# Performance work log

Measured on AMD Instinct MI355X. Metric: run time of the kernel, lower is better.

## Reference

```python
import jax, jax.numpy as jnp
import numpy as np

HIDDEN = 2048
NUM_HEADS = 6
HEAD_V = 512          # head_dim * expand_v = 256 * 2
VALUE_DIM = NUM_HEADS * HEAD_V  # 3072
CONV_K = 4
PHASE_BASE = 10000.0
EPS = 1e-5


def _causal_depthwise_conv(x, w):
    # x: [B, T, C], w: [C, K]; causal depthwise conv, no bias, no activation
    B, T, C = x.shape
    K = w.shape[1]
    xp = jnp.pad(x, ((0, 0), (K - 1, 0), (0, 0)))
    y = jnp.zeros_like(x)
    for j in range(K):
        y = y + xp[:, j:j + T, :] * w[:, j]
    return y


def _rotate(x, ang):
    # x: [..., D] interleaved RoPE pairs, ang: [..., D//2] pair angles
    cos = jnp.cos(ang)
    sin = jnp.sin(ang)
    xe = x[..., ::2]
    xo = x[..., 1::2]
    ye = xe * cos - xo * sin
    yo = xo * cos + xe * sin
    return jnp.stack([ye, yo], axis=-1).reshape(x.shape)


def setup_inputs() -> dict:
    key = jax.random.key(0)
    ks = jax.random.split(key, 12)
    s = 0.02
    return {
        "hidden_states": jax.random.normal(ks[0], (2, 2048, HIDDEN), jnp.float32),
        "Wq": jax.random.normal(ks[1], (HIDDEN, VALUE_DIM), jnp.float32) * s,
        "Wk": jax.random.normal(ks[2], (HIDDEN, VALUE_DIM), jnp.float32) * s,
        "Wv": jax.random.normal(ks[3], (HIDDEN, VALUE_DIM), jnp.float32) * s,
        "Wa": jax.random.normal(ks[4], (HIDDEN, NUM_HEADS), jnp.float32) * s,
        "Wb": jax.random.normal(ks[5], (HIDDEN, NUM_HEADS), jnp.float32) * s,
        "Wg": jax.random.normal(ks[6], (HIDDEN, VALUE_DIM), jnp.float32) * s,
        "Wo": jax.random.normal(ks[7], (VALUE_DIM, HIDDEN), jnp.float32) * s,
        "conv_q": jax.random.normal(ks[8], (VALUE_DIM, CONV_K), jnp.float32) * s,
        "conv_k": jax.random.normal(ks[9], (VALUE_DIM, CONV_K), jnp.float32) * s,
        "conv_v": jax.random.normal(ks[10], (VALUE_DIM, CONV_K), jnp.float32) * s,
        "rms_w": jnp.ones((HEAD_V,), jnp.float32),
    }


def _forward(hidden_states, Wq, Wk, Wv, Wa, Wb, Wg, Wo, conv_q, conv_k, conv_v, rms_w):
    B, T, _ = hidden_states.shape
    H, D = NUM_HEADS, HEAD_V
    inv_freq = 1.0 / (PHASE_BASE ** (jnp.arange(0, D, 2, dtype=jnp.float32) / D))  # [D/2]

    q = _causal_depthwise_conv(hidden_states @ Wq, conv_q).reshape(B, T, H, D)
    k = _causal_depthwise_conv(hidden_states @ Wk, conv_k).reshape(B, T, H, D)
    v = _causal_depthwise_conv(hidden_states @ Wv, conv_v).reshape(B, T, H, D)

    # pair angles (RoPE-style): raw even channels scaled by inverse frequencies
    theta = q[..., ::2] * inv_freq           # [B, T, H, D/2] output/query phase
    psi = k[..., ::2] * inv_freq             # write phase
    # state rotation per step = phase increment so cumulative state phase tracks theta
    phi = theta - jnp.concatenate([jnp.zeros_like(theta[:, :1]), theta[:, :-1]], axis=1)

    alpha = jax.nn.sigmoid(hidden_states @ Wa)  # [B, T, H] decay gate
    beta = jax.nn.sigmoid(hidden_states @ Wb)   # [B, T, H] write gate

    # time-major scan inputs
    tm = lambda a: jnp.moveaxis(a, 1, 0)
    xs = (tm(theta), tm(psi), tm(phi), tm(v), tm(alpha), tm(beta))

    def step(state, inp):
        th, ps, ph, vt, at, bt = inp  # state: [B, H, D]
        retained = _rotate(state, ph) * at[..., None]
        write = _rotate(vt, ps)
        new_state = retained + bt[..., None] * write
        out_t = _rotate(new_state, -th)
        return new_state, out_t

    state0 = jnp.zeros((B, H, D), hidden_states.dtype)
    _, out = jax.lax.scan(step, state0, xs)     # out: [T, B, H, D]
    out = jnp.moveaxis(out, 0, 1)               # [B, T, H, D]

    # gated RMSNorm over head_v_dim, then output projection
    g = (hidden_states @ Wg).reshape(B, T, H, D)
    rms = jax.lax.rsqrt(jnp.mean(jnp.square(out), axis=-1, keepdims=True) + EPS)
    o = out * rms * rms_w * jax.nn.silu(g)
    return (o.reshape(B, T, VALUE_DIM) @ Wo)


def reference(hidden_states, Wq, Wk, Wv, Wa, Wb, Wg, Wo, conv_q, conv_k, conv_v, rms_w):
    return _forward(hidden_states, Wq, Wk, Wv, Wa, Wb, Wg, Wo, conv_q, conv_k, conv_v, rms_w)
```

## Files before the change

kernel.cpp:

```cpp
#include <hip/hip_runtime.h>
#include <hip/hip_bf16.h>
#include <stdint.h>

using bf16 = __hip_bfloat16;
using mfrag = __attribute__((ext_vector_type(8))) __bf16;
using f32x4 = __attribute__((ext_vector_type(4))) float;

#define TOKENS 4096
#define HID    2048
#define VD     3072
#define NH     6
#define HD     512
#define NPAIR  256
#define N1     9216
#define NC     64
#define CHUNK  32

__device__ __forceinline__ void gld_lds16(const bf16* g, bf16* l) {
    __builtin_amdgcn_global_load_lds((const __attribute__((address_space(1))) void*)g,
                                     (__attribute__((address_space(3))) void*)l, 16, 0, 0);
}

#define VMWAIT(n) asm volatile("s_waitcnt vmcnt(" #n ")" ::: "memory")
#define SCHED0    __builtin_amdgcn_sched_barrier(0)
#define SBAR      __builtin_amdgcn_s_barrier()

template<int BN_T>
__global__ __launch_bounds__(512, 2) void k_gemm4(const bf16* __restrict__ A,
                                                  const bf16* __restrict__ Bt,
                                                  void* __restrict__ Cv,
                                                  int M, int N, int K, int obf,
                                                  int n0, int nbn) {
    constexpr int WN   = (BN_T == 256) ? 4 : 2;
    constexpr int WM   = 8 / WN;
    constexpr int MF   = (256 / WM) / 16;
    constexpr int AQ   = MF / 4;
    constexpr int SH   = AQ * 16;
    constexpr int NHT  = 2 + BN_T / 128;
    constexpr int HT   = 16384;
    constexpr int SLOT = NHT * HT;

    extern __shared__ char smem[];
    const int tid  = threadIdx.x;
    const int wave = tid >> 6;
    const int lane = tid & 63;
    const int lrow = lane & 15;
    const int lk   = lane >> 4;
    const int wm   = wave / WN;
    const int wn   = wave % WN;

    const int bid = blockIdx.x;
    const int xcd = bid & 7;
    const int kk2 = bid >> 3;
    const int rn  = nbn >> 1;
    const int jj  = kk2 & 31;
    const int bm  = ((((xcd >> 1) << 2) + (jj & 3)) << 8);
    const int bn  = ((xcd & 1) * rn + (kk2 >> 5) * 8 + (jj >> 2)) * BN_T;

    const int NT = K >> 6;

    auto ST_B = [&](int half, int t) {
        char* sb = smem + (size_t)(t & 1) * SLOT + (2 + half) * HT;
        const int ko = t << 6;
#pragma unroll
        for (int i = 0; i < 2; ++i) {
            const int L = i * 512 + tid;
            const int r = L >> 3;
            const int c = (L & 7) ^ (r & 7);
            gld_lds16(Bt + (size_t)(bn + half * 128 + r) * K + ko + c * 8,
                      (bf16*)(sb + (size_t)L * 16));
        }
    };
    auto ST_A = [&](int unit, int t) {
        char* sb = smem + (size_t)(t & 1) * SLOT;
        const int ko = t << 6;
        const int s  = tid / (SH * 8);
        const int W  = tid % (SH * 8);
        const int rl = W >> 3;
        const int c  = W & 7;
        const int r256 = s * (256 / WM) + unit * SH + rl;
        const int cl = c ^ (r256 & 7);
        const int ht = r256 >> 7, lr = r256 & 127;
        gld_lds16(A + (size_t)(bm + r256) * K + ko + cl * 8,
                  (bf16*)(sb + (size_t)ht * HT + (size_t)lr * 128 + c * 16));
    };

    auto rdA = [&](const char* rb, int mf, int kk) -> mfrag {
        const int r  = wm * (MF * 16) + mf * 16 + lrow;
        const int ht = r >> 7, lr = r & 127;
        const int cc = (kk * 4 + lk) ^ (lr & 7);
        return *(const mfrag*)(rb + (size_t)ht * HT + (size_t)lr * 128 + cc * 16);
    };
    auto rdB = [&](const char* rb, int nf, int kk) -> mfrag {
        const int r  = wn * 64 + nf * 16 + lrow;
        const int ht = r >> 7, lr = r & 127;
        const int cc = (kk * 4 + lk) ^ (lr & 7);
        return *(const mfrag*)(rb + (size_t)(2 + ht) * HT + (size_t)lr * 128 + cc * 16);
    };

    f32x4 acc[MF][4];
#pragma unroll
    for (int m = 0; m < MF; ++m)
#pragma unroll
        for (int n = 0; n < 4; ++n) acc[m][n] = f32x4{0.f, 0.f, 0.f, 0.f};

    ST_B(0, 0);
    if (BN_T == 256) ST_B(1, 0);
    ST_A(0, 0); ST_A(1, 0); ST_A(2, 0); ST_A(3, 0);

#define MFMA_PHASE(q)                                                              \
    {                                                                              \
        mfrag af[AQ][2];                                                           \
        _Pragma("unroll")                                                          \
        for (int i = 0; i < AQ; ++i)                                               \
            _Pragma("unroll")                                                      \
            for (int kx = 0; kx < 2; ++kx) af[i][kx] = rdA(rb, (q) * AQ + i, kx);  \
        SCHED0;                                                                    \
        __builtin_amdgcn_s_setprio(1);                                             \
        _Pragma("unroll")                                                          \
        for (int i = 0; i < AQ; ++i)                                               \
            _Pragma("unroll")                                                      \
            for (int nf = 0; nf < 4; ++nf) {                                       \
                const int mi = (q) * AQ + i;                                       \
                acc[mi][nf] = __builtin_amdgcn_mfma_f32_16x16x32_bf16(af[i][0], bfr[nf][0], acc[mi][nf], 0, 0, 0); \
                acc[mi][nf] = __builtin_amdgcn_mfma_f32_16x16x32_bf16(af[i][1], bfr[nf][1], acc[mi][nf], 0, 0, 0); \
            }                                                                      \
        __builtin_amdgcn_s_setprio(0);                                             \
    }

    for (int kt = 0; kt < NT; ++kt) {
        const char* rb = smem + (size_t)(kt & 1) * SLOT;
        const bool last = (kt == NT - 1);
        mfrag bfr[4][2];

        VMWAIT(3);
        SCHED0; SBAR;
#pragma unroll
        for (int nf = 0; nf < 4; ++nf)
#pragma unroll
            for (int kx = 0; kx < 2; ++kx) bfr[nf][kx] = rdB(rb, nf, kx);
        if (!last) ST_B(0, kt + 1);
        MFMA_PHASE(0)

        if (last) { VMWAIT(2); } else { VMWAIT(4); }
        SCHED0; SBAR;
        if (!last) {
            if (BN_T == 256) ST_B(1, kt + 1);
            else             { ST_A(0, kt + 1); ST_A(1, kt + 1); }
        }
        MFMA_PHASE(1)

        if (last) { VMWAIT(1); } else { VMWAIT(5); }
        SCHED0; SBAR;
        if (!last) {
            if (BN_T == 256) { ST_A(0, kt + 1); ST_A(1, kt + 1); }
            else             { ST_A(2, kt + 1); ST_A(3, kt + 1); }
        }
        MFMA_PHASE(2)

        if (last) { VMWAIT(0); } else { VMWAIT(6); }
        SCHED0; SBAR;
        if (!last && BN_T == 256) { ST_A(2, kt + 1); ST_A(3, kt + 1); }
        MFMA_PHASE(3)
    }
#undef MFMA_PHASE

#pragma unroll
    for (int m = 0; m < MF; ++m)
#pragma unroll
        for (int j2 = 0; j2 < 4; ++j2) {
            const int r = bm + wm * (MF * 16) + m * 16 + lk * 4 + j2;
#pragma unroll
            for (int n = 0; n < 4; ++n) {
                const int c = n0 + bn + wn * 64 + n * 16 + lrow;
                if (obf) ((bf16*)Cv)[(size_t)r * N + c] = __float2bfloat16(acc[m][n][j2]);
                else     ((float*)Cv)[(size_t)r * N + c] = acc[m][n][j2];
            }
        }
}

__global__ void k_prep_w(const float* __restrict__ Wq, const float* __restrict__ Wk,
                         const float* __restrict__ Wv, const float* __restrict__ Wg,
                         bf16* __restrict__ Wt) {
    __shared__ float t[32][33];
    const int n0 = blockIdx.x * 32;
    const int k0 = blockIdx.y * 32;
    const int tx = threadIdx.x, ty = threadIdx.y;
    const float* src; int cb, cs;
    if (n0 < 1536)      { int m = n0;        src = Wq; cb = (m >> 8) * 512 + (m & 255) * 2; cs = 2; }
    else if (n0 < 3072) { int m = n0 - 1536; src = Wk; cb = (m >> 8) * 512 + (m & 255) * 2; cs = 2; }
    else if (n0 < 6144) { int m = n0 - 3072; src = Wv; cb = m; cs = 1; }
    else                { int m = n0 - 6144; src = Wg; cb = m; cs = 1; }
#pragma unroll
    for (int i = 0; i < 4; ++i) {
        int k = k0 + ty + i * 8;
        t[ty + i * 8][tx] = src[(size_t)k * VD + cb + cs * tx];
    }
    __syncthreads();
#pragma unroll
    for (int i = 0; i < 4; ++i) {
        int n = n0 + ty + i * 8;
        Wt[(size_t)n * HID + k0 + tx] = __float2bfloat16(t[tx][ty + i * 8]);
    }
}

__global__ void k_tr_cast(const float* __restrict__ src, bf16* __restrict__ dst, int R, int Ccol) {
    __shared__ float t[32][33];
    const int c0 = blockIdx.x * 32, r0 = blockIdx.y * 32;
    const int tx = threadIdx.x, ty = threadIdx.y;
#pragma unroll
    for (int i = 0; i < 4; ++i)
        t[ty + i * 8][tx] = src[(size_t)(r0 + ty + i * 8) * Ccol + c0 + tx];
    __syncthreads();
#pragma unroll
    for (int i = 0; i < 4; ++i)
        dst[(size_t)(c0 + ty + i * 8) * R + r0 + tx] = __float2bfloat16(t[tx][ty + i * 8]);
}

__global__ __launch_bounds__(256) void k_ab(const float* __restrict__ hs, const float* __restrict__ Wa,
                                            const float* __restrict__ Wb,
                                            float* __restrict__ alpha, float* __restrict__ beta,
                                            bf16* __restrict__ hsb) {
    const int tok = blockIdx.x;
    const int tid = threadIdx.x;
    float part[12];
#pragma unroll
    for (int j = 0; j < 12; ++j) part[j] = 0.f;
    const float* hrow = hs + (size_t)tok * HID;
    bf16* hbrow = hsb + (size_t)tok * HID;
    for (int i = 0; i < 8; ++i) {
        int k = i * 256 + tid;
        float x = hrow[k];
        hbrow[k] = __float2bfloat16(x);
        const float* wa = Wa + k * NH;
        const float* wb = Wb + k * NH;
#pragma unroll
        for (int j = 0; j < NH; ++j) {
            part[j]     = fmaf(x, wa[j], part[j]);
            part[6 + j] = fmaf(x, wb[j], part[6 + j]);
        }
    }
    __shared__ float red[12][4];
    const int lane = tid & 63, wv = tid >> 6;
#pragma unroll
    for (int j = 0; j < 12; ++j) {
        float s = part[j];
        for (int off = 32; off; off >>= 1) s += __shfl_down(s, off);
        if (lane == 0) red[j][wv] = s;
    }
    __syncthreads();
    if (tid < 12) {
        float s = red[tid][0] + red[tid][1] + red[tid][2] + red[tid][3];
        float v = 1.f / (1.f + expf(-s));
        if (tid < 6) alpha[(size_t)tok * NH + tid] = v;
        else         beta [(size_t)tok * NH + tid - 6] = v;
    }
}

__global__ __launch_bounds__(256) void k_scan1(const bf16* __restrict__ X,
                                               const float* __restrict__ alpha,
                                               const float* __restrict__ beta,
                                               const float* __restrict__ cq,
                                               const float* __restrict__ ck,
                                               const float* __restrict__ cv,
                                               float* __restrict__ U, float* __restrict__ pp) {
    const int bx = blockIdx.x;
    const int c  = bx % NC;
    const int h  = (bx / NC) % NH;
    const int b  = bx / (NC * NH);
    const int p  = threadIdx.x;
    const int t0 = c * CHUNK;
    const int ch2 = h * HD + 2 * p;
    const float wq0 = cq[ch2 * 4 + 0], wq1 = cq[ch2 * 4 + 1], wq2 = cq[ch2 * 4 + 2], wq3 = cq[ch2 * 4 + 3];
    const float wk0 = ck[ch2 * 4 + 0], wk1 = ck[ch2 * 4 + 1], wk2 = ck[ch2 * 4 + 2], wk3 = ck[ch2 * 4 + 3];
    const float wa0 = cv[ch2 * 4 + 0], wa1 = cv[ch2 * 4 + 1], wa2 = cv[ch2 * 4 + 2], wa3 = cv[ch2 * 4 + 3];
    const float wb0 = cv[(ch2 + 1) * 4 + 0], wb1 = cv[(ch2 + 1) * 4 + 1],
                wb2 = cv[(ch2 + 1) * 4 + 2], wb3 = cv[(ch2 + 1) * 4 + 3];
    const float invf = exp2f(-13.287712379549449f * ((float)p * (1.0f / 256.0f)));
    const int qcol = h * NPAIR + p;
    const int kcol = 1536 + h * NPAIR + p;
    const int vcol = 3072 + ch2;

    float xq[3], xk[3], xv0[3], xv1[3];
#pragma unroll
    for (int i = 0; i < 3; ++i) {
        int t = t0 - 3 + i;
        if (t >= 0) {
            size_t tok = (size_t)b * 2048 + t;
            const bf16* xr = X + tok * N1;
            xq[i] = __bfloat162float(xr[qcol]);
            xk[i] = __bfloat162float(xr[kcol]);
            __hip_bfloat162 vv = *(const __hip_bfloat162*)&xr[vcol];
            xv0[i] = __bfloat162float(vv.x);
            xv1[i] = __bfloat162float(vv.y);
        } else { xq[i] = xk[i] = xv0[i] = xv1[i] = 0.f; }
    }

    float u0 = 0.f, u1 = 0.f, ap = 1.f;
    for (int t = t0; t < t0 + CHUNK; ++t) {
        const size_t tok = (size_t)b * 2048 + t;
        const bf16* xr = X + tok * N1;
        float nq = __bfloat162float(xr[qcol]);
        float nk = __bfloat162float(xr[kcol]);
        __hip_bfloat162 vv = *(const __hip_bfloat162*)&xr[vcol];
        float nv0 = __bfloat162float(vv.x);
        float nv1 = __bfloat162float(vv.y);
        float yq  = wq3 * nq  + wq2 * xq[2]  + wq1 * xq[1]  + wq0 * xq[0];
        float yk  = wk3 * nk  + wk2 * xk[2]  + wk1 * xk[1]  + wk0 * xk[0];
        float yv0 = wa3 * nv0 + wa2 * xv0[2] + wa1 * xv0[1] + wa0 * xv0[0];
        float yv1 = wb3 * nv1 + wb2 * xv1[2] + wb1 * xv1[1] + wb0 * xv1[0];
        xq[0] = xq[1]; xq[1] = xq[2]; xq[2] = nq;
        xk[0] = xk[1]; xk[1] = xk[2]; xk[2] = nk;
        xv0[0] = xv0[1]; xv0[1] = xv0[2]; xv0[2] = nv0;
        xv1[0] = xv1[1]; xv1[1] = xv1[2]; xv1[2] = nv1;
        float theta = yq * invf, psi = yk * invf;
        float d = psi - theta, sn, cs;
        __sincosf(d, &sn, &cs);
        float w0 = yv0 * cs - yv1 * sn;
        float w1 = yv1 * cs + yv0 * sn;
        float a  = alpha[tok * NH + h];
        float bb = beta [tok * NH + h];
        u0 = fmaf(a, u0, bb * w0);
        u1 = fmaf(a, u1, bb * w1);
        ap *= a;
        *(float2*)&U[tok * (size_t)VD + h * HD + 2 * p] = float2{u0, u1};
        if (p == 0) pp[tok * NH + h] = ap;
    }
}

__global__ __launch_bounds__(512) void k_carry(const float* __restrict__ U, const float* __restrict__ pp,
                                               float* __restrict__ carry) {
    const int bh = blockIdx.x;
    const int b = bh / NH, h = bh % NH;
    const int d = threadIdx.x;
    float ue[NC], pv[NC];
#pragma unroll
    for (int c = 0; c < NC; ++c) {
        size_t tok = (size_t)b * 2048 + c * CHUNK + CHUNK - 1;
        ue[c] = U[tok * (size_t)VD + h * HD + d];
        pv[c] = pp[tok * NH + h];
    }
    float s = 0.f;
#pragma unroll
    for (int c = 0; c < NC; ++c) {
        carry[((size_t)bh * NC + c) * HD + d] = s;
        s = ue[c] + pv[c] * s;
    }
}

__global__ __launch_bounds__(256) void k_pass3(const float* __restrict__ U, const float* __restrict__ pp,
                                               const float* __restrict__ carry, const bf16* __restrict__ X,
                                               const float* __restrict__ rms_w, bf16* __restrict__ O) {
    const int bx = blockIdx.x;
    const int h = bx % NH;
    const size_t tok = bx / NH;
    const int b = (int)(tok >> 11);
    const int t = (int)(tok & 2047);
    const int c = t / CHUNK;
    const int tid = threadIdx.x;
    const int d = tid * 2;
    float2 uu = *(const float2*)&U[tok * (size_t)VD + h * HD + d];
    float  P  = pp[tok * NH + h];
    float2 cy = *(const float2*)&carry[((size_t)(b * NH + h) * NC + c) * HD + d];
    float u0 = fmaf(P, cy.x, uu.x);
    float u1 = fmaf(P, cy.y, uu.y);
    float s = u0 * u0 + u1 * u1;
    for (int off = 32; off; off >>= 1) s += __shfl_down(s, off);
    __shared__ float r4[4];
    const int lane = tid & 63, wv = tid >> 6;
    if (lane == 0) r4[wv] = s;
    __syncthreads();
    float tot = r4[0] + r4[1] + r4[2] + r4[3];
    float rms = rsqrtf(tot * (1.f / 512.f) + 1e-5f);
    __hip_bfloat162 gg = *(const __hip_bfloat162*)&X[tok * N1 + 6144 + h * HD + d];
    float g0 = __bfloat162float(gg.x), g1 = __bfloat162float(gg.y);
    float si0 = g0 / (1.f + expf(-g0));
    float si1 = g1 / (1.f + expf(-g1));
    float o0 = u0 * rms * rms_w[d]     * si0;
    float o1 = u1 * rms * rms_w[d + 1] * si1;
    __hip_bfloat162 ob;
    ob.x = __float2bfloat16(o0);
    ob.y = __float2bfloat16(o1);
    *(__hip_bfloat162*)&O[tok * (size_t)VD + h * HD + d] = ob;
}

extern "C" void kernel_launch(void* const* d_in, const int* in_sizes, int n_in,
                              void* d_out, int out_size, void* d_ws, size_t ws_size,
                              hipStream_t stream) {
    const float* hs   = (const float*)d_in[0];
    const float* Wq   = (const float*)d_in[1];
    const float* Wk   = (const float*)d_in[2];
    const float* Wv   = (const float*)d_in[3];
    const float* Wa   = (const float*)d_in[4];
    const float* Wb   = (const float*)d_in[5];
    const float* Wg   = (const float*)d_in[6];
    const float* Wo   = (const float*)d_in[7];
    const float* cq   = (const float*)d_in[8];
    const float* ck   = (const float*)d_in[9];
    const float* cv   = (const float*)d_in[10];
    const float* rmsw = (const float*)d_in[11];

    char* ws = (char*)d_ws;
    size_t off = 0;
    auto alloc = [&](size_t bytes) -> void* {
        void* p = ws + off;
        off = (off + bytes + 255) & ~(size_t)255;
        return p;
    };
    bf16*  hsb   = (bf16*) alloc((size_t)TOKENS * HID * 2);
    bf16*  Wt    = (bf16*) alloc((size_t)N1 * HID * 2);
    bf16*  Wot   = (bf16*) alloc((size_t)HID * VD * 2);
    bf16*  X     = (bf16*) alloc((size_t)TOKENS * N1 * 2);
    float* U     = (float*)alloc((size_t)TOKENS * VD * 4);
    float* alp   = (float*)alloc((size_t)TOKENS * NH * 4);
    float* bet   = (float*)alloc((size_t)TOKENS * NH * 4);
    float* pp    = (float*)alloc((size_t)TOKENS * NH * 4);
    float* carry = (float*)alloc((size_t)2 * NH * NC * HD * 4);
    bf16*  O     = (bf16*)Wt;

    hipFuncSetAttribute((const void*)k_gemm4<256>,
                        hipFuncAttributeMaxDynamicSharedMemorySize, 2 * 4 * 16384);
    hipFuncSetAttribute((const void*)k_gemm4<128>,
                        hipFuncAttributeMaxDynamicSharedMemorySize, 2 * 3 * 16384);

    k_prep_w<<<dim3(N1 / 32, HID / 32), dim3(32, 8), 0, stream>>>(Wq, Wk, Wv, Wg, Wt);
    k_tr_cast<<<dim3(HID / 32, VD / 32), dim3(32, 8), 0, stream>>>(Wo, Wot, VD, HID);
    k_ab<<<TOKENS, 256, 0, stream>>>(hs, Wa, Wb, alp, bet, hsb);
    k_gemm4<256><<<dim3(512), 512, 2 * 4 * 16384, stream>>>(hsb, Wt, X, TOKENS, N1, HID, 1, 0, 32);
    k_gemm4<128><<<dim3(128), 512, 2 * 3 * 16384, stream>>>(hsb, Wt + (size_t)8192 * HID, X,
                                                            TOKENS, N1, HID, 1, 8192, 8);
    k_scan1<<<2 * NH * NC, 256, 0, stream>>>(X, alp, bet, cq, ck, cv, U, pp);
    k_carry<<<2 * NH, 512, 0, stream>>>(U, pp, carry);
    k_pass3<<<TOKENS * NH, 256, 0, stream>>>(U, pp, carry, X, rmsw, O);
    k_gemm4<128><<<dim3(256), 512, 2 * 3 * 16384, stream>>>(O, Wot, d_out, TOKENS, HID, VD, 0, 0, 16);
}
```

Measured before the change: 335.6 us.

## Prefetch next A fragments during MFMA phases and store scan intermediate in bf16

The GEMM main loop now reads the A fragments for the next quarter from LDS before issuing the current quarter's MFMAs, so LDS reads overlap matrix math. The vmcnt waits are tightened to match, and one barrier/wait in the last phase is dropped. Separately, the scan intermediate U is stored as bf16 instead of fp32, halving its write and read traffic in scan1, carry and pass3. The cost is more live registers for the extra fragment buffers, which could cause spills under launch bounds 512x2, plus reduced precision of the intra-chunk scan values. The changed waits also carry a risk of LDS hazards if the counts are wrong.

```diff
diff --git a/kernel.cpp b/kernel.cpp
--- a/kernel.cpp
+++ b/kernel.cpp
@@ -26,7 +26,7 @@
 #define SBAR      __builtin_amdgcn_s_barrier()
 
 template<int BN_T>
-__global__ __launch_bounds__(512, 2) void k_gemm4(const bf16* __restrict__ A,
+__global__ __launch_bounds__(512, 2) void k_gemm5(const bf16* __restrict__ A,
                                                   const bf16* __restrict__ Bt,
                                                   void* __restrict__ Cv,
                                                   int M, int N, int K, int obf,
@@ -108,62 +108,69 @@
     if (BN_T == 256) ST_B(1, 0);
     ST_A(0, 0); ST_A(1, 0); ST_A(2, 0); ST_A(3, 0);
 
-#define MFMA_PHASE(q)                                                              \
-    {                                                                              \
-        mfrag af[AQ][2];                                                           \
-        _Pragma("unroll")                                                          \
-        for (int i = 0; i < AQ; ++i)                                               \
-            _Pragma("unroll")                                                      \
-            for (int kx = 0; kx < 2; ++kx) af[i][kx] = rdA(rb, (q) * AQ + i, kx);  \
-        SCHED0;                                                                    \
-        __builtin_amdgcn_s_setprio(1);                                             \
-        _Pragma("unroll")                                                          \
-        for (int i = 0; i < AQ; ++i)                                               \
-            _Pragma("unroll")                                                      \
-            for (int nf = 0; nf < 4; ++nf) {                                       \
-                const int mi = (q) * AQ + i;                                       \
-                acc[mi][nf] = __builtin_amdgcn_mfma_f32_16x16x32_bf16(af[i][0], bfr[nf][0], acc[mi][nf], 0, 0, 0); \
-                acc[mi][nf] = __builtin_amdgcn_mfma_f32_16x16x32_bf16(af[i][1], bfr[nf][1], acc[mi][nf], 0, 0, 0); \
-            }                                                                      \
-        __builtin_amdgcn_s_setprio(0);                                             \
-    }
+#define RD_A(AF, band)                                                          \
+    _Pragma("unroll")                                                           \
+    for (int i = 0; i < AQ; ++i)                                                \
+        _Pragma("unroll")                                                       \
+        for (int kx = 0; kx < 2; ++kx) AF[i][kx] = rdA(rb, (band) * AQ + i, kx);
+
+#define MFMA_Q(q, AF)                                                           \
+    __builtin_amdgcn_s_setprio(1);                                              \
+    _Pragma("unroll")                                                           \
+    for (int i = 0; i < AQ; ++i)                                                \
+        _Pragma("unroll")                                                       \
+        for (int nf = 0; nf < 4; ++nf) {                                        \
+            const int mi = (q) * AQ + i;                                        \
+            acc[mi][nf] = __builtin_amdgcn_mfma_f32_16x16x32_bf16(AF[i][0], bfr[nf][0], acc[mi][nf], 0, 0, 0); \
+            acc[mi][nf] = __builtin_amdgcn_mfma_f32_16x16x32_bf16(AF[i][1], bfr[nf][1], acc[mi][nf], 0, 0, 0); \
+        }                                                                       \
+    __builtin_amdgcn_s_setprio(0);
 
     for (int kt = 0; kt < NT; ++kt) {
         const char* rb = smem + (size_t)(kt & 1) * SLOT;
         const bool last = (kt == NT - 1);
         mfrag bfr[4][2];
-
-        VMWAIT(3);
+        mfrag af0[AQ][2], af1[AQ][2], af2[AQ][2], af3[AQ][2];
+
+        VMWAIT(2);
         SCHED0; SBAR;
 #pragma unroll
         for (int nf = 0; nf < 4; ++nf)
 #pragma unroll
             for (int kx = 0; kx < 2; ++kx) bfr[nf][kx] = rdB(rb, nf, kx);
+        RD_A(af0, 0)
         if (!last) ST_B(0, kt + 1);
-        MFMA_PHASE(0)
-
-        if (last) { VMWAIT(2); } else { VMWAIT(4); }
+        RD_A(af1, 1)
+        SCHED0;
+        MFMA_Q(0, af0)
+
+        if (last) { VMWAIT(1); } else { VMWAIT(3); }
         SCHED0; SBAR;
         if (!last) {
             if (BN_T == 256) ST_B(1, kt + 1);
             else             { ST_A(0, kt + 1); ST_A(1, kt + 1); }
         }
-        MFMA_PHASE(1)
-
-        if (last) { VMWAIT(1); } else { VMWAIT(5); }
+        RD_A(af2, 2)
+        SCHED0;
+        MFMA_Q(1, af1)
+
+        if (last) { VMWAIT(0); } else { VMWAIT(4); }
         SCHED0; SBAR;
         if (!last) {
             if (BN_T == 256) { ST_A(0, kt + 1); ST_A(1, kt + 1); }
             else             { ST_A(2, kt + 1); ST_A(3, kt + 1); }
         }
-        MFMA_PHASE(2)
-
-        if (last) { VMWAIT(0); } else { VMWAIT(6); }
-        SCHED0; SBAR;
+        RD_A(af3, 3)
+        SCHED0;
+        MFMA_Q(2, af2)
+
+        SBAR;
         if (!last && BN_T == 256) { ST_A(2, kt + 1); ST_A(3, kt + 1); }
-        MFMA_PHASE(3)
-    }
-#undef MFMA_PHASE
+        SCHED0;
+        MFMA_Q(3, af3)
+    }
+#undef RD_A
+#undef MFMA_Q
 
 #pragma unroll
     for (int m = 0; m < MF; ++m)
@@ -263,7 +270,7 @@
                                                const float* __restrict__ cq,
                                                const float* __restrict__ ck,
                                                const float* __restrict__ cv,
-                                               float* __restrict__ U, float* __restrict__ pp) {
+                                               bf16* __restrict__ U, float* __restrict__ pp) {
     const int bx = blockIdx.x;
     const int c  = bx % NC;
     const int h  = (bx / NC) % NH;
@@ -323,12 +330,15 @@
         u0 = fmaf(a, u0, bb * w0);
         u1 = fmaf(a, u1, bb * w1);
         ap *= a;
-        *(float2*)&U[tok * (size_t)VD + h * HD + 2 * p] = float2{u0, u1};
+        __hip_bfloat162 us;
+        us.x = __float2bfloat16(u0);
+        us.y = __float2bfloat16(u1);
+        *(__hip_bfloat162*)&U[tok * (size_t)VD + h * HD + 2 * p] = us;
         if (p == 0) pp[tok * NH + h] = ap;
     }
 }
 
-__global__ __launch_bounds__(512) void k_carry(const float* __restrict__ U, const float* __restrict__ pp,
+__global__ __launch_bounds__(512) void k_carry(const bf16* __restrict__ U, const float* __restrict__ pp,
                                                float* __restrict__ carry) {
     const int bh = blockIdx.x;
     const int b = bh / NH, h = bh % NH;
@@ -337,7 +347,7 @@
 #pragma unroll
     for (int c = 0; c < NC; ++c) {
         size_t tok = (size_t)b * 2048 + c * CHUNK + CHUNK - 1;
-        ue[c] = U[tok * (size_t)VD + h * HD + d];
+        ue[c] = __bfloat162float(U[tok * (size_t)VD + h * HD + d]);
         pv[c] = pp[tok * NH + h];
     }
     float s = 0.f;
@@ -348,7 +358,7 @@
     }
 }
 
-__global__ __launch_bounds__(256) void k_pass3(const float* __restrict__ U, const float* __restrict__ pp,
+__global__ __launch_bounds__(256) void k_pass3(const bf16* __restrict__ U, const float* __restrict__ pp,
                                                const float* __restrict__ carry, const bf16* __restrict__ X,
                                                const float* __restrict__ rms_w, bf16* __restrict__ O) {
     const int bx = blockIdx.x;
@@ -359,11 +369,11 @@
     const int c = t / CHUNK;
     const int tid = threadIdx.x;
     const int d = tid * 2;
-    float2 uu = *(const float2*)&U[tok * (size_t)VD + h * HD + d];
+    __hip_bfloat162 uu2 = *(const __hip_bfloat162*)&U[tok * (size_t)VD + h * HD + d];
     float  P  = pp[tok * NH + h];
     float2 cy = *(const float2*)&carry[((size_t)(b * NH + h) * NC + c) * HD + d];
-    float u0 = fmaf(P, cy.x, uu.x);
-    float u1 = fmaf(P, cy.y, uu.y);
+    float u0 = fmaf(P, cy.x, __bfloat162float(uu2.x));
+    float u1 = fmaf(P, cy.y, __bfloat162float(uu2.y));
     float s = u0 * u0 + u1 * u1;
     for (int off = 32; off; off >>= 1) s += __shfl_down(s, off);
     __shared__ float r4[4];
@@ -411,26 +421,26 @@
     bf16*  Wt    = (bf16*) alloc((size_t)N1 * HID * 2);
     bf16*  Wot   = (bf16*) alloc((size_t)HID * VD * 2);
     bf16*  X     = (bf16*) alloc((size_t)TOKENS * N1 * 2);
-    float* U     = (float*)alloc((size_t)TOKENS * VD * 4);
+    bf16*  U     = (bf16*) alloc((size_t)TOKENS * VD * 2);
     float* alp   = (float*)alloc((size_t)TOKENS * NH * 4);
     float* bet   = (float*)alloc((size_t)TOKENS * NH * 4);
     float* pp    = (float*)alloc((size_t)TOKENS * NH * 4);
     float* carry = (float*)alloc((size_t)2 * NH * NC * HD * 4);
     bf16*  O     = (bf16*)Wt;
 
-    hipFuncSetAttribute((const void*)k_gemm4<256>,
+    hipFuncSetAttribute((const void*)k_gemm5<256>,
                         hipFuncAttributeMaxDynamicSharedMemorySize, 2 * 4 * 16384);
-    hipFuncSetAttribute((const void*)k_gemm4<128>,
+    hipFuncSetAttribute((const void*)k_gemm5<128>,
                         hipFuncAttributeMaxDynamicSharedMemorySize, 2 * 3 * 16384);
 
     k_prep_w<<<dim3(N1 / 32, HID / 32), dim3(32, 8), 0, stream>>>(Wq, Wk, Wv, Wg, Wt);
     k_tr_cast<<<dim3(HID / 32, VD / 32), dim3(32, 8), 0, stream>>>(Wo, Wot, VD, HID);
     k_ab<<<TOKENS, 256, 0, stream>>>(hs, Wa, Wb, alp, bet, hsb);
-    k_gemm4<256><<<dim3(512), 512, 2 * 4 * 16384, stream>>>(hsb, Wt, X, TOKENS, N1, HID, 1, 0, 32);
-    k_gemm4<128><<<dim3(128), 512, 2 * 3 * 16384, stream>>>(hsb, Wt + (size_t)8192 * HID, X,
+    k_gemm5<256><<<dim3(512), 512, 2 * 4 * 16384, stream>>>(hsb, Wt, X, TOKENS, N1, HID, 1, 0, 32);
+    k_gemm5<128><<<dim3(128), 512, 2 * 3 * 16384, stream>>>(hsb, Wt + (size_t)8192 * HID, X,
                                                             TOKENS, N1, HID, 1, 8192, 8);
     k_scan1<<<2 * NH * NC, 256, 0, stream>>>(X, alp, bet, cq, ck, cv, U, pp);
     k_carry<<<2 * NH, 512, 0, stream>>>(U, pp, carry);
     k_pass3<<<TOKENS * NH, 256, 0, stream>>>(U, pp, carry, X, rmsw, O);
-    k_gemm4<128><<<dim3(256), 512, 2 * 3 * 16384, stream>>>(O, Wot, d_out, TOKENS, HID, VD, 0, 0, 16);
-}
+    k_gemm5<128><<<dim3(256), 512, 2 * 3 * 16384, stream>>>(O, Wot, d_out, TOKENS, HID, VD, 0, 0, 16);
+}
```

Result: slower. 343.6 us (+2.4%).
